# Kernel tuning notes

Hardware: AMD Instinct MI355X
Metric: run time of the kernel (lower is better)

Reference implementation:

```python
import jax, jax.numpy as jnp
import numpy as np

DIM = 1024
D_STATE = 16
D_CONV = 4
EXPAND = 2
D_INNER = EXPAND * DIM          # 2048
DT_RANK = (DIM + 15) // 16      # 64 (math.ceil(d_model/16))
BSZ = 2
SEQ = 2048


def setup_inputs() -> dict:
    key = jax.random.key(0)
    ks = jax.random.split(key, 8)
    g = lambda k, shape, scale: (jax.random.normal(k, shape, jnp.float32) * scale)
    return {
        "x": g(ks[0], (BSZ, SEQ, DIM), 1.0),
        # in_proj: Linear(d_model -> 2*d_inner, bias=False)
        "W_in": g(ks[1], (2 * D_INNER, DIM), DIM ** -0.5),
        # depthwise causal conv1d: groups=d_inner, kernel d_conv, bias=True
        "conv_w": g(ks[2], (D_INNER, 1, D_CONV), D_CONV ** -0.5),
        "conv_b": jnp.zeros((D_INNER,), jnp.float32),
        # x_proj: Linear(d_inner -> dt_rank + 2*d_state, bias=False)
        "W_xproj": g(ks[3], (DT_RANK + 2 * D_STATE, D_INNER), D_INNER ** -0.5),
        # dt_proj: Linear(dt_rank -> d_inner, bias=True)
        "W_dt": g(ks[4], (D_INNER, DT_RANK), DT_RANK ** -0.5),
        "b_dt": g(ks[5], (D_INNER,), 0.1),
        # S4D-real init: A = -exp(A_log), A_log = log(1..d_state)
        "A_log": jnp.log(jnp.broadcast_to(
            jnp.arange(1, D_STATE + 1, dtype=jnp.float32), (D_INNER, D_STATE))),
        "D": jnp.ones((D_INNER,), jnp.float32),
        # out_proj: Linear(d_inner -> d_model, bias=False)
        "W_out": g(ks[6], (DIM, D_INNER), D_INNER ** -0.5),
        # wrapper LayerNorm(dim)
        "gamma": jnp.ones((DIM,), jnp.float32),
        "beta": jnp.zeros((DIM,), jnp.float32),
    }


def reference(x, W_in, conv_w, conv_b, W_xproj, W_dt, b_dt,
              A_log, D, W_out, gamma, beta):
    B, L, _ = x.shape
    # ---- input projection, split into conv path and gate ----
    xz = x @ W_in.T                              # (B, L, 2*d_inner)
    xc, z = jnp.split(xz, 2, axis=-1)
    # ---- depthwise causal conv1d + SiLU ----
    xt = jnp.transpose(xc, (0, 2, 1))            # (B, d_inner, L)
    conv = jax.lax.conv_general_dilated(
        xt, conv_w, window_strides=(1,), padding=[(D_CONV - 1, 0)],
        dimension_numbers=("NCH", "OIH", "NCH"), feature_group_count=D_INNER)
    u = jax.nn.silu(jnp.transpose(conv + conv_b[None, :, None], (0, 2, 1)))  # (B,L,d_inner)
    # ---- input-dependent delta, B, C ----
    xdbc = u @ W_xproj.T                          # (B, L, dt_rank + 2*d_state)
    dt = xdbc[..., :DT_RANK]
    Bm = xdbc[..., DT_RANK:DT_RANK + D_STATE]     # (B, L, d_state)
    Cm = xdbc[..., DT_RANK + D_STATE:]            # (B, L, d_state)
    delta = jax.nn.softplus(dt @ W_dt.T + b_dt)   # (B, L, d_inner)
    A = -jnp.exp(A_log)                           # (d_inner, d_state)
    # ---- selective scan: h_t = exp(dt*A) h_{t-1} + dt*B_t*u_t ; y_t = <h_t, C_t> ----
    def step(h, inputs):
        d_t, u_t, B_t, C_t = inputs               # (B,d_inner),(B,d_inner),(B,S),(B,S)
        dA = jnp.exp(d_t[:, :, None] * A)         # (B, d_inner, S)
        h = h * dA + (d_t * u_t)[:, :, None] * B_t[:, None, :]
        y = jnp.einsum("bds,bs->bd", h, C_t)
        return h, y
    tm = lambda a: jnp.transpose(a, (1, 0, 2))    # time-major for scan
    h0 = jnp.zeros((B, D_INNER, D_STATE), x.dtype)
    _, ys = jax.lax.scan(step, h0, (tm(delta), tm(u), tm(Bm), tm(Cm)))
    y = jnp.transpose(ys, (1, 0, 2)) + u * D      # skip term D*u
    y = y * jax.nn.silu(z)                        # gate
    out = y @ W_out.T                             # (B, L, dim)
    # ---- wrapper LayerNorm(dim), eps=1e-5 ----
    mean = out.mean(-1, keepdims=True)
    var = out.var(-1, keepdims=True)
    return (out - mean) * jax.lax.rsqrt(var + 1e-5) * gamma + beta
```

## Files before the change

### kernel.cpp

```cpp
#include <hip/hip_runtime.h>
#include <stdint.h>

typedef unsigned short u16;
typedef __bf16 bf16x8 __attribute__((ext_vector_type(8)));
typedef unsigned short u16x8 __attribute__((ext_vector_type(8)));
typedef unsigned short u16x4 __attribute__((ext_vector_type(4)));
typedef float f32x4 __attribute__((ext_vector_type(4)));

#define BSZ 2
#define SEQ 2048
#define DIM 1024
#define D_INNER 2048
#define DT_RANK 64
#define D_STATE 16
#define XPROJ_N 96
#define NCHUNK 32
#define CHUNK_T 64
#define LOG2E 1.44269504f

#define N_X   4194304
#define N_W   4194304
#define N_WX  196608
#define N_WDT 131072
#define N_WO  2097152
#define N_XD  393216

__device__ __forceinline__ float bf2f(u16 h) {
    return __uint_as_float(((unsigned)h) << 16);
}
__device__ __forceinline__ u16 f2bf(float f) {
    unsigned u = __float_as_uint(f);
    unsigned r = (u + 0x7FFFu + ((u >> 16) & 1u)) >> 16;
    return (u16)r;
}

__device__ __forceinline__ f32x4 mfma16(bf16x8 a, bf16x8 b, f32x4 c) {
    return __builtin_amdgcn_mfma_f32_16x16x32_bf16(a, b, c, 0, 0, 0);
}

__device__ __forceinline__ void gload_lds16(const void* g, void* l) {
    __builtin_amdgcn_global_load_lds(
        (const __attribute__((address_space(1))) unsigned int*)(uintptr_t)g,
        (__attribute__((address_space(3))) unsigned int*)(uintptr_t)l,
        16, 0, 0);
}

__device__ __forceinline__ void split4(const float* __restrict__ in,
                                       u16* __restrict__ hi, u16* __restrict__ lo,
                                       long i)
{
    f32x4 v = *(const f32x4*)(in + i);
    u16x4 h, l;
    #pragma unroll
    for (int j = 0; j < 4; j++) {
        u16 hh = f2bf(v[j]);
        h[j] = hh;
        l[j] = f2bf(v[j] - bf2f(hh));
    }
    *(u16x4*)(hi + i) = h;
    *(u16x4*)(lo + i) = l;
}

__global__ __launch_bounds__(256)
void megasplit4(const float* __restrict__ x,  u16* __restrict__ xh,  u16* __restrict__ xl,
                const float* __restrict__ w,  u16* __restrict__ wh,  u16* __restrict__ wl,
                const float* __restrict__ wx, u16* __restrict__ wxh, u16* __restrict__ wxl,
                const float* __restrict__ wd, u16* __restrict__ wdh, u16* __restrict__ wdl)
{
    long i = ((long)blockIdx.x * 256 + threadIdx.x) * 4;
    if (i < N_X) { split4(x, xh, xl, i); return; }
    i -= N_X;
    if (i < N_W) { split4(w, wh, wl, i); return; }
    i -= N_W;
    if (i < N_WX) { split4(wx, wxh, wxl, i); return; }
    i -= N_WX;
    if (i < N_WDT) { split4(wd, wdh, wdl, i); }
}

__global__ __launch_bounds__(512, 2)
void gemm256_xz(const u16* __restrict__ xh, const u16* __restrict__ xl,
                const u16* __restrict__ wh, const u16* __restrict__ wl,
                u16* __restrict__ xc, float* __restrict__ z)
{
    __shared__ u16 lds[49152];

    const int tid  = threadIdx.x;
    const int w    = tid >> 6;
    const int lane = tid & 63;
    const int r16  = lane & 15;
    const int quad = lane >> 4;
    const int wr   = w >> 2;
    const int wc   = w & 3;
    const long m0  = (long)blockIdx.y * 256;
    const long n0  = (long)blockIdx.x * 256;

    const int c0 = tid, c1 = tid + 512;
    const int ma0 = c0 >> 2, kc0 = ((c0 & 3) ^ ((ma0 >> 1) & 3)) * 8;
    const int ma1 = c1 >> 2, kc1 = ((c1 & 3) ^ ((ma1 >> 1) & 3)) * 8;
    const int arow0 = ((int)m0 + ma0) * DIM + kc0;
    const int arow1 = ((int)m0 + ma1) * DIM + kc1;
    const int brow0 = ((int)n0 + ma0) * DIM + kc0;
    const int brow1 = ((int)n0 + ma1) * DIM + kc1;

    int caof[8], cbof[4];
    #pragma unroll
    for (int i = 0; i < 8; i++) {
        int m = wr * 128 + i * 16 + r16;
        caof[i] = (m * 4 + (quad ^ ((m >> 1) & 3))) * 8;
    }
    #pragma unroll
    for (int j = 0; j < 4; j++) {
        int n = wc * 64 + j * 16 + r16;
        cbof[j] = (n * 4 + (quad ^ ((n >> 1) & 3))) * 8;
    }

    f32x4 acc[8][4];
    #pragma unroll
    for (int i = 0; i < 8; i++)
        #pragma unroll
        for (int j = 0; j < 4; j++) acc[i][j] = {0.f, 0.f, 0.f, 0.f};

    gload_lds16(xh + arow0,      lds + c0 * 8);
    gload_lds16(xh + arow1,      lds + c1 * 8);
    gload_lds16(wh + brow0,      lds + 24576 + c0 * 8);
    gload_lds16(wh + brow1,      lds + 24576 + c1 * 8);
    gload_lds16(xh + arow0 + 32, lds + 8192 + c0 * 8);
    gload_lds16(xh + arow1 + 32, lds + 8192 + c1 * 8);
    gload_lds16(wh + brow0 + 32, lds + 24576 + 8192 + c0 * 8);
    gload_lds16(wh + brow1 + 32, lds + 24576 + 8192 + c1 * 8);
    asm volatile("s_waitcnt vmcnt(4)" ::: "memory");
    __builtin_amdgcn_s_barrier();

    int kt = 0;
#define XZ_ITER(CUR, SL)                                                      \
  {                                                                           \
    int st = kt + 2; if (st > 95) st = 95;                                    \
    const int ts = st >> 5;                                                   \
    const int kb = (st & 31) * 32;                                            \
    const u16* As = (ts < 2) ? xh : xl;                                       \
    const u16* Bs = (ts == 1) ? wl : wh;                                      \
    const u16* Alds = lds + (CUR) * 8192;                                     \
    const u16* Blds = lds + 24576 + (CUR) * 8192;                             \
      \
    bf16x8 bfr[4], afr[4];                                                    \
    _Pragma("unroll") for (int j = 0; j < 4; j++)                             \
        bfr[j] = *(const bf16x8*)(Blds + cbof[j]);                            \
    _Pragma("unroll") for (int i = 0; i < 4; i++)                             \
        afr[i] = *(const bf16x8*)(Alds + caof[i]);                            \
    gload_lds16(As + arow0 + kb, lds + (SL) * 8192 + c0 * 8);                 \
    gload_lds16(As + arow1 + kb, lds + (SL) * 8192 + c1 * 8);                 \
    __builtin_amdgcn_sched_barrier(0);                                        \
    __builtin_amdgcn_s_barrier();                                             \
    asm volatile("s_waitcnt lgkmcnt(0)" ::: "memory");                        \
    __builtin_amdgcn_sched_barrier(0);                                        \
    __builtin_amdgcn_s_setprio(1);                                            \
    _Pragma("unroll") for (int i = 0; i < 4; i++)                             \
      _Pragma("unroll") for (int j = 0; j < 4; j++)                           \
        acc[i][j] = mfma16(afr[i], bfr[j], acc[i][j]);                        \
    __builtin_amdgcn_s_setprio(0);                                            \
    __builtin_amdgcn_sched_barrier(0);                                        \
    __builtin_amdgcn_s_barrier();                                             \
            \
    bf16x8 af2[4];                                                            \
    _Pragma("unroll") for (int i = 0; i < 4; i++)                             \
        af2[i] = *(const bf16x8*)(Alds + caof[4 + i]);                        \
    gload_lds16(Bs + brow0 + kb, lds + 24576 + (SL) * 8192 + c0 * 8);         \
    gload_lds16(Bs + brow1 + kb, lds + 24576 + (SL) * 8192 + c1 * 8);         \
    __builtin_amdgcn_sched_barrier(0);                                        \
    __builtin_amdgcn_s_barrier();                                             \
    asm volatile("s_waitcnt lgkmcnt(0)" ::: "memory");                        \
    __builtin_amdgcn_sched_barrier(0);                                        \
    __builtin_amdgcn_s_setprio(1);                                            \
    _Pragma("unroll") for (int i = 0; i < 4; i++)                             \
      _Pragma("unroll") for (int j = 0; j < 4; j++)                           \
        acc[4 + i][j] = mfma16(af2[i], bfr[j], acc[4 + i][j]);                \
    __builtin_amdgcn_s_setprio(0);                                            \
    __builtin_amdgcn_sched_barrier(0);                                        \
    asm volatile("s_waitcnt vmcnt(4)" ::: "memory");                          \
    __builtin_amdgcn_s_barrier();                                             \
    kt++;                                                                     \
  }

    #pragma unroll 1
    for (int it = 0; it < 32; it++) {
        XZ_ITER(0, 2)
        XZ_ITER(1, 0)
        XZ_ITER(2, 1)
    }
#undef XZ_ITER

    asm volatile("s_waitcnt vmcnt(0)" ::: "memory");

    const bool isz = (n0 >= 2048);
    #pragma unroll
    for (int i = 0; i < 8; i++) {
        #pragma unroll
        for (int j = 0; j < 4; j++) {
            long col = n0 + wc * 64 + j * 16 + r16;
            #pragma unroll
            for (int r = 0; r < 4; r++) {
                long row = m0 + wr * 128 + i * 16 + quad * 4 + r;
                if (!isz) xc[row * (long)D_INNER + col] = f2bf(acc[i][j][r]);
                else      z[row * (long)D_INNER + (col - D_INNER)] = acc[i][j][r];
            }
        }
    }
}

__global__ __launch_bounds__(256)
void gemm128_sk2(const u16* __restrict__ Ah, int lda,
                 const u16* __restrict__ Bh, const u16* __restrict__ Bl, int ldb,
                 float* __restrict__ OutBase, int ldc, int K0)
{
    __shared__ u16 lds[12288];
    u16* Ah_l = lds;
    u16* Bh_l = lds + 4096;
    u16* Bl_l = lds + 8192;

    const int tid  = threadIdx.x;
    const int w    = tid >> 6;
    const int lane = tid & 63;
    const int r16  = lane & 15;
    const int quad = lane >> 4;
    const int wr   = w >> 1;
    const int wc   = w & 1;
    const long m0  = (long)blockIdx.y * 128;
    const long n0  = (long)blockIdx.x * 128;
    const int kbase = blockIdx.z * K0;
    float* Out = OutBase + (long)blockIdx.z * 4194304;

    const int c0 = w * 64 + lane;
    const int c1 = 256 + c0;
    const int ma0 = c0 >> 2, kca0 = ((c0 & 3) ^ ((ma0 >> 1) & 3)) * 8;
    const int ma1 = c1 >> 2, kca1 = ((c1 & 3) ^ ((ma1 >> 1) & 3)) * 8;

    const u16* Arow0 = Ah + (m0 + ma0) * (long)lda + kbase + kca0;
    const u16* Arow1 = Ah + (m0 + ma1) * (long)lda + kbase + kca1;
    const u16* Brow0 = Bh + (n0 + ma0) * (long)ldb + kbase + kca0;
    const u16* Brow1 = Bh + (n0 + ma1) * (long)ldb + kbase + kca1;
    const u16* Blrow0 = Bl + (n0 + ma0) * (long)ldb + kbase + kca0;
    const u16* Blrow1 = Bl + (n0 + ma1) * (long)ldb + kbase + kca1;

    f32x4 acc[4][4];
    #pragma unroll
    for (int i = 0; i < 4; i++)
        #pragma unroll
        for (int j = 0; j < 4; j++) acc[i][j] = {0.f, 0.f, 0.f, 0.f};

    int caof[4], cbof[4];
    #pragma unroll
    for (int i = 0; i < 4; i++) {
        int m = wr * 64 + i * 16 + r16;
        caof[i] = (m * 4 + (quad ^ ((m >> 1) & 3))) * 8;
        int n = wc * 64 + i * 16 + r16;
        cbof[i] = (n * 4 + (quad ^ ((n >> 1) & 3))) * 8;
    }

    for (int k0 = 0; k0 < K0; k0 += 32) {
        __syncthreads();
        gload_lds16(Arow0 + k0, Ah_l + c0 * 8);
        gload_lds16(Arow1 + k0, Ah_l + c1 * 8);
        gload_lds16(Brow0 + k0, Bh_l + c0 * 8);
        gload_lds16(Brow1 + k0, Bh_l + c1 * 8);
        gload_lds16(Blrow0 + k0, Bl_l + c0 * 8);
        gload_lds16(Blrow1 + k0, Bl_l + c1 * 8);
        __syncthreads();

        bf16x8 fah[4], fbh[4], fbl[4];
        #pragma unroll
        for (int i = 0; i < 4; i++) {
            fah[i] = *(const bf16x8*)(Ah_l + caof[i]);
            fbh[i] = *(const bf16x8*)(Bh_l + cbof[i]);
            fbl[i] = *(const bf16x8*)(Bl_l + cbof[i]);
        }
        #pragma unroll
        for (int i = 0; i < 4; i++) {
            #pragma unroll
            for (int j = 0; j < 4; j++) {
                acc[i][j] = mfma16(fah[i], fbh[j], acc[i][j]);
                acc[i][j] = mfma16(fah[i], fbl[j], acc[i][j]);
            }
        }
    }

    #pragma unroll
    for (int i = 0; i < 4; i++) {
        #pragma unroll
        for (int j = 0; j < 4; j++) {
            long col = n0 + wc * 64 + j * 16 + r16;
            #pragma unroll
            for (int r = 0; r < 4; r++) {
                long row = m0 + wr * 64 + i * 16 + quad * 4 + r;
                Out[row * (long)ldc + col] = acc[i][j][r];
            }
        }
    }
}

__global__ __launch_bounds__(64)
void gemm_dt32(const u16* __restrict__ Ah, const u16* __restrict__ Al, int lda,
               const u16* __restrict__ Bh, const u16* __restrict__ Bl, int ldb,
               float* __restrict__ C, int ldc, const float* __restrict__ bias)
{
    const int lane = threadIdx.x;
    const int r16  = lane & 15;
    const int quad = lane >> 4;
    const long m0 = (long)blockIdx.y * 32;
    const long n0 = (long)blockIdx.x * 32;

    const u16* Ah0 = Ah + (m0 + r16) * (long)lda + quad * 8;
    const u16* Ah1 = Ah0 + 16L * lda;
    const u16* Al0 = Al + (m0 + r16) * (long)lda + quad * 8;
    const u16* Al1 = Al0 + 16L * lda;
    const u16* Bh0 = Bh + (n0 + r16) * (long)ldb + quad * 8;
    const u16* Bh1 = Bh0 + 16L * ldb;
    const u16* Bl0 = Bl + (n0 + r16) * (long)ldb + quad * 8;
    const u16* Bl1 = Bl0 + 16L * ldb;

    f32x4 acc00 = {0,0,0,0}, acc01 = {0,0,0,0}, acc10 = {0,0,0,0}, acc11 = {0,0,0,0};

    #pragma unroll
    for (int k = 0; k < DT_RANK; k += 32) {
        bf16x8 a0h = *(const bf16x8*)(Ah0 + k);
        bf16x8 a1h = *(const bf16x8*)(Ah1 + k);
        bf16x8 a0l = *(const bf16x8*)(Al0 + k);
        bf16x8 a1l = *(const bf16x8*)(Al1 + k);
        bf16x8 b0h = *(const bf16x8*)(Bh0 + k);
        bf16x8 b1h = *(const bf16x8*)(Bh1 + k);
        bf16x8 b0l = *(const bf16x8*)(Bl0 + k);
        bf16x8 b1l = *(const bf16x8*)(Bl1 + k);
        acc00 = mfma16(a0h, b0h, acc00); acc00 = mfma16(a0h, b0l, acc00); acc00 = mfma16(a0l, b0h, acc00);
        acc01 = mfma16(a0h, b1h, acc01); acc01 = mfma16(a0h, b1l, acc01); acc01 = mfma16(a0l, b1h, acc01);
        acc10 = mfma16(a1h, b0h, acc10); acc10 = mfma16(a1h, b0l, acc10); acc10 = mfma16(a1l, b0h, acc10);
        acc11 = mfma16(a1h, b1h, acc11); acc11 = mfma16(a1h, b1l, acc11); acc11 = mfma16(a1l, b1h, acc11);
    }

    #pragma unroll
    for (int i = 0; i < 2; i++) {
        #pragma unroll
        for (int j = 0; j < 2; j++) {
            f32x4 v = (i == 0) ? (j == 0 ? acc00 : acc01) : (j == 0 ? acc10 : acc11);
            long col = n0 + j * 16 + r16;
            #pragma unroll
            for (int r = 0; r < 4; r++) {
                long row = m0 + i * 16 + quad * 4 + r;
                float x = v[r] + bias[col];
                x = (x > 15.f) ? x : log1pf(__expf(x));
                C[row * (long)ldc + col] = x;
            }
        }
    }
}

__global__ __launch_bounds__(64)
void gemm3_skp(const u16* __restrict__ A, int lda,
               const u16* __restrict__ Bh, const u16* __restrict__ Bl, int ldb,
               float* __restrict__ Cpart, int ldc, int K0)
{
    const int lane = threadIdx.x;
    const int r16  = lane & 15;
    const int quad = lane >> 4;
    const long m0 = (long)blockIdx.y * 32;
    const long n0 = (long)blockIdx.x * 32;
    const int kbase = blockIdx.z * K0;
    float* C = Cpart + (long)blockIdx.z * N_XD;

    const u16* Ap0 = A  + (m0 + r16) * (long)lda + quad * 8 + kbase;
    const u16* Ap1 = Ap0 + 16L * lda;
    const u16* Bh0 = Bh + (n0 + r16) * (long)ldb + quad * 8 + kbase;
    const u16* Bh1 = Bh0 + 16L * ldb;
    const u16* Bl0 = Bl + (n0 + r16) * (long)ldb + quad * 8 + kbase;
    const u16* Bl1 = Bl0 + 16L * ldb;

    f32x4 acc00 = {0,0,0,0}, acc01 = {0,0,0,0}, acc10 = {0,0,0,0}, acc11 = {0,0,0,0};

    for (int k = 0; k < K0; k += 32) {
        bf16x8 a0 = *(const bf16x8*)(Ap0 + k);
        bf16x8 a1 = *(const bf16x8*)(Ap1 + k);
        bf16x8 b0h = *(const bf16x8*)(Bh0 + k);
        bf16x8 b1h = *(const bf16x8*)(Bh1 + k);
        bf16x8 b0l = *(const bf16x8*)(Bl0 + k);
        bf16x8 b1l = *(const bf16x8*)(Bl1 + k);
        acc00 = mfma16(a0, b0h, acc00); acc00 = mfma16(a0, b0l, acc00);
        acc01 = mfma16(a0, b1h, acc01); acc01 = mfma16(a0, b1l, acc01);
        acc10 = mfma16(a1, b0h, acc10); acc10 = mfma16(a1, b0l, acc10);
        acc11 = mfma16(a1, b1h, acc11); acc11 = mfma16(a1, b1l, acc11);
    }

    #pragma unroll
    for (int i = 0; i < 2; i++) {
        #pragma unroll
        for (int j = 0; j < 2; j++) {
            f32x4 v = (i == 0) ? (j == 0 ? acc00 : acc01) : (j == 0 ? acc10 : acc11);
            long col = n0 + j * 16 + r16;
            #pragma unroll
            for (int r = 0; r < 4; r++) {
                long row = m0 + i * 16 + quad * 4 + r;
                C[row * (long)ldc + col] = v[r];
            }
        }
    }
}

__global__ __launch_bounds__(256)
void combine3(const float* __restrict__ part, float* __restrict__ xdbc,
              u16* __restrict__ hi, u16* __restrict__ lo)
{
    long i = ((long)blockIdx.x * 256 + threadIdx.x) * 4;
    if (i >= N_XD) return;
    f32x4 s = *(const f32x4*)(part + i);
    #pragma unroll
    for (int j = 1; j < 8; j++) {
        f32x4 p = *(const f32x4*)(part + (long)j * N_XD + i);
        s[0] += p[0]; s[1] += p[1]; s[2] += p[2]; s[3] += p[3];
    }
    *(f32x4*)(xdbc + i) = s;
    u16x4 h, l;
    #pragma unroll
    for (int j = 0; j < 4; j++) {
        u16 hh = f2bf(s[j]);
        h[j] = hh;
        l[j] = f2bf(s[j] - bf2f(hh));
    }
    *(u16x4*)(hi + i) = h;
    *(u16x4*)(lo + i) = l;
}

__global__ __launch_bounds__(256)
void conv_silu(const u16* __restrict__ xc, const float* __restrict__ cw,
               const float* __restrict__ cb, u16* __restrict__ u)
{
    long idx = ((long)blockIdx.x * 256 + threadIdx.x) * 8;
    int t  = (int)((idx >> 11) & 2047);
    int d0 = (int)(idx & 2047);

    bf16x8 xrow[4];
    #pragma unroll
    for (int j = 0; j < 4; j++) {
        int tt = t - 3 + j;
        if (tt >= 0) xrow[j] = *(const bf16x8*)(xc + idx + (long)(j - 3) * D_INNER);
        else         xrow[j] = bf16x8{0,0,0,0,0,0,0,0};
    }
    u16x8 out;
    #pragma unroll
    for (int e = 0; e < 8; e++) {
        int d = d0 + e;
        float acc = cb[d];
        #pragma unroll
        for (int j = 0; j < 4; j++)
            acc += cw[d * 4 + j] * (float)xrow[j][e];
        out[e] = f2bf(acc / (1.f + __expf(-acc)));
    }
    *(u16x8*)(u + idx) = out;
}

__global__ __launch_bounds__(256)
void scan_partA(const float* __restrict__ delta, const u16* __restrict__ u,
                const float* __restrict__ xdbc, const float* __restrict__ A_log,
                float* __restrict__ hbuf, float* __restrict__ sdelta,
                const float* __restrict__ wout, u16* __restrict__ wouth,
                u16* __restrict__ woutl)
{
    const int d = blockIdx.x * 256 + threadIdx.x;
    const int c = blockIdx.y;
    const int b = blockIdx.z;
    const int t0 = c * CHUNK_T;

    float Af[16];
    #pragma unroll
    for (int s = 0; s < 16; s++) Af[s] = -__expf(A_log[d * 16 + s]) * LOG2E;

    float h[16];
    #pragma unroll
    for (int s = 0; s < 16; s++) h[s] = 0.f;
    float sd = 0.f;

    const float* dptr = delta + ((long)b * SEQ + t0) * D_INNER + d;
    const u16*   uptr = u     + ((long)b * SEQ + t0) * D_INNER + d;
    const float* xp   = xdbc  + ((long)b * SEQ + t0) * XPROJ_N;

    for (int t = 0; t < CHUNK_T; t++) {
        float dl = dptr[(long)t * D_INNER];
        float uu = bf2f(uptr[(long)t * D_INNER]);
        f32x4 B0 = *(const f32x4*)(xp + t * XPROJ_N + DT_RANK);
        f32x4 B1 = *(const f32x4*)(xp + t * XPROJ_N + DT_RANK + 4);
        f32x4 B2 = *(const f32x4*)(xp + t * XPROJ_N + DT_RANK + 8);
        f32x4 B3 = *(const f32x4*)(xp + t * XPROJ_N + DT_RANK + 12);
        float Bv[16] = {B0[0],B0[1],B0[2],B0[3], B1[0],B1[1],B1[2],B1[3],
                        B2[0],B2[1],B2[2],B2[3], B3[0],B3[1],B3[2],B3[3]};
        sd += dl;
        float dlu = dl * uu;
        #pragma unroll
        for (int s = 0; s < 16; s++)
            h[s] = h[s] * exp2f(dl * Af[s]) + dlu * Bv[s];
    }

    float* hout = hbuf + ((long)(b * NCHUNK + c) * D_INNER + d) * 16;
    #pragma unroll
    for (int s = 0; s < 16; s++) hout[s] = h[s];
    sdelta[(long)(b * NCHUNK + c) * D_INNER + d] = sd;

    long tidg = (((long)b * NCHUNK + c) * 8 + blockIdx.x) * 256 + threadIdx.x;
    long base = tidg * 16;
    #pragma unroll
    for (int k = 0; k < 4; k++) split4(wout, wouth, woutl, base + 4 * k);
}

__global__ __launch_bounds__(256)
void scan_fixup(float* __restrict__ hbuf, const float* __restrict__ sdelta,
                const float* __restrict__ A_log)
{
    const int idx = blockIdx.x * 256 + threadIdx.x;
    const int ds = idx & (D_INNER * 16 - 1);
    const int b  = idx >> 15;
    const float Af = -__expf(A_log[ds]) * LOG2E;
    float hin = 0.f;
    #pragma unroll 4
    for (int c = 0; c < NCHUNK; c++) {
        long gi = (long)(b * NCHUNK + c) * (D_INNER * 16) + ds;
        float e = hbuf[gi];
        hbuf[gi] = hin;
        float sd = sdelta[(long)(b * NCHUNK + c) * D_INNER + (ds >> 4)];
        hin = e + exp2f(Af * sd) * hin;
    }
}

__global__ __launch_bounds__(256)
void scan_partC(const float* __restrict__ delta, const u16* __restrict__ u,
                const float* __restrict__ xdbc, const float* __restrict__ z,
                const float* __restrict__ A_log, const float* __restrict__ Dp,
                const float* __restrict__ hbuf, u16* __restrict__ y)
{
    const int d = blockIdx.x * 256 + threadIdx.x;
    const int c = blockIdx.y;
    const int b = blockIdx.z;
    const int t0 = c * CHUNK_T;

    float Af[16];
    #pragma unroll
    for (int s = 0; s < 16; s++) Af[s] = -__expf(A_log[d * 16 + s]) * LOG2E;
    const float Dd = Dp[d];

    float h[16];
    const float* hin = hbuf + ((long)(b * NCHUNK + c) * D_INNER + d) * 16;
    #pragma unroll
    for (int s = 0; s < 16; s++) h[s] = hin[s];

    const float* dptr = delta + ((long)b * SEQ + t0) * D_INNER + d;
    const u16*   uptr = u     + ((long)b * SEQ + t0) * D_INNER + d;
    const float* zptr = z     + ((long)b * SEQ + t0) * D_INNER + d;
    const float* xp   = xdbc  + ((long)b * SEQ + t0) * XPROJ_N;
    u16* yptr = y + ((long)b * SEQ + t0) * D_INNER + d;

    for (int t = 0; t < CHUNK_T; t++) {
        float dl = dptr[(long)t * D_INNER];
        float uu = bf2f(uptr[(long)t * D_INNER]);
        float zl = zptr[(long)t * D_INNER];
        f32x4 B0 = *(const f32x4*)(xp + t * XPROJ_N + DT_RANK);
        f32x4 B1 = *(const f32x4*)(xp + t * XPROJ_N + DT_RANK + 4);
        f32x4 B2 = *(const f32x4*)(xp + t * XPROJ_N + DT_RANK + 8);
        f32x4 B3 = *(const f32x4*)(xp + t * XPROJ_N + DT_RANK + 12);
        f32x4 C0 = *(const f32x4*)(xp + t * XPROJ_N + DT_RANK + 16);
        f32x4 C1 = *(const f32x4*)(xp + t * XPROJ_N + DT_RANK + 20);
        f32x4 C2 = *(const f32x4*)(xp + t * XPROJ_N + DT_RANK + 24);
        f32x4 C3 = *(const f32x4*)(xp + t * XPROJ_N + DT_RANK + 28);
        float Bv[16] = {B0[0],B0[1],B0[2],B0[3], B1[0],B1[1],B1[2],B1[3],
                        B2[0],B2[1],B2[2],B2[3], B3[0],B3[1],B3[2],B3[3]};
        float Cv[16] = {C0[0],C0[1],C0[2],C0[3], C1[0],C1[1],C1[2],C1[3],
                        C2[0],C2[1],C2[2],C2[3], C3[0],C3[1],C3[2],C3[3]};
        float dlu = dl * uu;
        float p0 = 0.f, p1 = 0.f, p2 = 0.f, p3 = 0.f;
        #pragma unroll
        for (int s = 0; s < 16; s += 4) {
            h[s]   = h[s]   * exp2f(dl * Af[s])   + dlu * Bv[s];
            h[s+1] = h[s+1] * exp2f(dl * Af[s+1]) + dlu * Bv[s+1];
            h[s+2] = h[s+2] * exp2f(dl * Af[s+2]) + dlu * Bv[s+2];
            h[s+3] = h[s+3] * exp2f(dl * Af[s+3]) + dlu * Bv[s+3];
            p0 += h[s]   * Cv[s];
            p1 += h[s+1] * Cv[s+1];
            p2 += h[s+2] * Cv[s+2];
            p3 += h[s+3] * Cv[s+3];
        }
        float acc = (p0 + p1) + (p2 + p3);
        float sz = zl / (1.f + __expf(-zl));
        float yy = (acc + uu * Dd) * sz;
        yptr[(long)t * D_INNER] = f2bf(yy);
    }
}

__global__ __launch_bounds__(256)
void layernorm_kernel(const float* __restrict__ pa, const float* __restrict__ pb,
                      const float* __restrict__ gamma, const float* __restrict__ beta,
                      float* __restrict__ out)
{
    const long row = blockIdx.x;
    const long base = row * DIM;
    int tid = threadIdx.x;
    float v[4];
    float sum = 0.f, sq = 0.f;
    #pragma unroll
    for (int i = 0; i < 4; i++) {
        long c = base + tid + i * 256;
        v[i] = pa[c] + pb[c];
        sum += v[i];
        sq  += v[i] * v[i];
    }
    #pragma unroll
    for (int off = 1; off < 64; off <<= 1) {
        sum += __shfl_xor(sum, off);
        sq  += __shfl_xor(sq, off);
    }
    __shared__ float ssum[4], ssq[4];
    int w = tid >> 6;
    if ((tid & 63) == 0) { ssum[w] = sum; ssq[w] = sq; }
    __syncthreads();
    float ts = ssum[0] + ssum[1] + ssum[2] + ssum[3];
    float tq = ssq[0] + ssq[1] + ssq[2] + ssq[3];
    float mean = ts * (1.f / DIM);
    float var  = tq * (1.f / DIM) - mean * mean;
    float rstd = rsqrtf(var + 1e-5f);
    float* o = out + base;
    #pragma unroll
    for (int i = 0; i < 4; i++) {
        int c = tid + i * 256;
        o[c] = (v[i] - mean) * rstd * gamma[c] + beta[c];
    }
}

extern "C" void kernel_launch(void* const* d_in, const int* in_sizes, int n_in,
                              void* d_out, int out_size, void* d_ws, size_t ws_size,
                              hipStream_t stream)
{
    const float* x      = (const float*)d_in[0];
    const float* W_in   = (const float*)d_in[1];
    const float* conv_w = (const float*)d_in[2];
    const float* conv_b = (const float*)d_in[3];
    const float* W_xproj= (const float*)d_in[4];
    const float* W_dt   = (const float*)d_in[5];
    const float* b_dt   = (const float*)d_in[6];
    const float* A_log  = (const float*)d_in[7];
    const float* Dv     = (const float*)d_in[8];
    const float* W_out  = (const float*)d_in[9];
    const float* gamma  = (const float*)d_in[10];
    const float* beta   = (const float*)d_in[11];

    char* ws = (char*)d_ws;
    u16*   xc    = (u16*)(ws);
    float* g3p   = (float*)(ws);
    u16*   xdh   = (u16*)(ws + 12582912);
    u16*   xdl   = (u16*)(ws + 14155776);
    float* hbuf  = (float*)(ws);
    u16*   wouth = (u16*)(ws + 8388608);
    u16*   woutl = (u16*)(ws + 12582912);
    float* z     = (float*)(ws + 16777216);
    float* opre  = (float*)(ws + 16777216);
    u16*   u     = (u16*)(ws + 50331648);
    u16*   xh    = (u16*)(ws + 67108864);
    u16*   xl    = (u16*)(ws + 75497472);
    u16*   wh    = (u16*)(ws + 83886080);
    u16*   wl    = (u16*)(ws + 92274688);
    float* delta = (float*)(ws + 67108864);
    float* xdbc  = (float*)(ws + 100663296);
    u16*   wxh   = (u16*)(ws + 102236160);
    u16*   wxl   = (u16*)(ws + 102629376);
    u16*   wdth  = (u16*)(ws + 103022592);
    u16*   wdtl  = (u16*)(ws + 103284736);
    float* sdel  = (float*)(ws + 103546880);
    u16*   yb    = (u16*)d_out;

    megasplit4<<<8512, 256, 0, stream>>>(x, xh, xl, W_in, wh, wl,
                                         W_xproj, wxh, wxl, W_dt, wdth, wdtl);
    gemm256_xz<<<dim3(16, 16), 512, 0, stream>>>(xh, xl, wh, wl, xc, z);
    conv_silu<<<4096, 256, 0, stream>>>(xc, conv_w, conv_b, u);
    gemm3_skp<<<dim3(3, 128, 8), 64, 0, stream>>>(
        u, D_INNER, wxh, wxl, D_INNER, g3p, XPROJ_N, 256);
    combine3<<<384, 256, 0, stream>>>(g3p, xdbc, xdh, xdl);
    gemm_dt32<<<dim3(64, 128), 64, 0, stream>>>(
        xdh, xdl, XPROJ_N, wdth, wdtl, DT_RANK, delta, D_INNER, b_dt);
    scan_partA<<<dim3(8, NCHUNK, BSZ), 256, 0, stream>>>(
        delta, u, xdbc, A_log, hbuf, sdel, W_out, wouth, woutl);
    scan_fixup<<<256, 256, 0, stream>>>(hbuf, sdel, A_log);
    scan_partC<<<dim3(8, NCHUNK, BSZ), 256, 0, stream>>>(delta, u, xdbc, z, A_log, Dv, hbuf, yb);
    gemm128_sk2<<<dim3(8, 32, 2), 256, 0, stream>>>(
        yb, D_INNER, wouth, woutl, D_INNER, opre, DIM, 1024);
    layernorm_kernel<<<4096, 256, 0, stream>>>(
        opre, opre + 4194304, gamma, beta, (float*)d_out);
}
```

Measured before the change: 442.3 us.

## Deepen xz GEMM LDS pipeline to four stages with register-prefetched fragments

The in_proj GEMM moves from a 3-stage to a 4-stage LDS ring buffer, prefetching three K-tiles ahead. It also double-buffers the B fragments and preloads the next tile's A fragments into registers during the current MFMA block, so LDS reads overlap compute. This is meant to hide global-load and LDS latency behind the MFMAs. The cost is 128KB of LDS and more registers, which may drop occupancy from 2 blocks per CU to 1.

```diff
diff --git a/kernel.cpp b/kernel.cpp
--- a/kernel.cpp
+++ b/kernel.cpp
@@ -82,7 +82,7 @@
                 const u16* __restrict__ wh, const u16* __restrict__ wl,
                 u16* __restrict__ xc, float* __restrict__ z)
 {
-    __shared__ u16 lds[49152];
+    __shared__ u16 lds[65536];
 
     const int tid  = threadIdx.x;
     const int w    = tid >> 6;
@@ -122,74 +122,82 @@
 
     gload_lds16(xh + arow0,      lds + c0 * 8);
     gload_lds16(xh + arow1,      lds + c1 * 8);
-    gload_lds16(wh + brow0,      lds + 24576 + c0 * 8);
-    gload_lds16(wh + brow1,      lds + 24576 + c1 * 8);
+    gload_lds16(wh + brow0,      lds + 32768 + c0 * 8);
+    gload_lds16(wh + brow1,      lds + 32768 + c1 * 8);
     gload_lds16(xh + arow0 + 32, lds + 8192 + c0 * 8);
     gload_lds16(xh + arow1 + 32, lds + 8192 + c1 * 8);
-    gload_lds16(wh + brow0 + 32, lds + 24576 + 8192 + c0 * 8);
-    gload_lds16(wh + brow1 + 32, lds + 24576 + 8192 + c1 * 8);
-    asm volatile("s_waitcnt vmcnt(4)" ::: "memory");
+    gload_lds16(wh + brow0 + 32, lds + 32768 + 8192 + c0 * 8);
+    gload_lds16(wh + brow1 + 32, lds + 32768 + 8192 + c1 * 8);
+    gload_lds16(xh + arow0 + 64, lds + 16384 + c0 * 8);
+    gload_lds16(xh + arow1 + 64, lds + 16384 + c1 * 8);
+    gload_lds16(wh + brow0 + 64, lds + 32768 + 16384 + c0 * 8);
+    gload_lds16(wh + brow1 + 64, lds + 32768 + 16384 + c1 * 8);
+    asm volatile("s_waitcnt vmcnt(8)" ::: "memory");
     __builtin_amdgcn_s_barrier();
 
+    bf16x8 aA[4], aB[4], bE[4], bO[4];
+    #pragma unroll
+    for (int j = 0; j < 4; j++) bE[j] = *(const bf16x8*)(lds + 32768 + cbof[j]);
+    #pragma unroll
+    for (int i = 0; i < 4; i++) aA[i] = *(const bf16x8*)(lds + caof[i]);
+
     int kt = 0;
-#define XZ_ITER(CUR, SL)                                                      \
+#define TILE_STEP(SC, SN, SS, BC, BN)                                         \
   {                                                                           \
-    int st = kt + 2; if (st > 95) st = 95;                                    \
+    int st = kt + 3; if (st > 95) st = 95;                                    \
     const int ts = st >> 5;                                                   \
     const int kb = (st & 31) * 32;                                            \
     const u16* As = (ts < 2) ? xh : xl;                                       \
     const u16* Bs = (ts == 1) ? wl : wh;                                      \
-    const u16* Alds = lds + (CUR) * 8192;                                     \
-    const u16* Blds = lds + 24576 + (CUR) * 8192;                             \
-      \
-    bf16x8 bfr[4], afr[4];                                                    \
-    _Pragma("unroll") for (int j = 0; j < 4; j++)                             \
-        bfr[j] = *(const bf16x8*)(Blds + cbof[j]);                            \
+    const u16* Ac = lds + (SC) * 8192;                                        \
+    const u16* An = lds + (SN) * 8192;                                        \
+    const u16* Bn = lds + 32768 + (SN) * 8192;                                \
+        \
+    asm volatile("s_waitcnt lgkmcnt(0)" ::: "memory");                        \
+    __builtin_amdgcn_sched_barrier(0);                                        \
     _Pragma("unroll") for (int i = 0; i < 4; i++)                             \
-        afr[i] = *(const bf16x8*)(Alds + caof[i]);                            \
-    gload_lds16(As + arow0 + kb, lds + (SL) * 8192 + c0 * 8);                 \
-    gload_lds16(As + arow1 + kb, lds + (SL) * 8192 + c1 * 8);                 \
-    __builtin_amdgcn_sched_barrier(0);                                        \
-    __builtin_amdgcn_s_barrier();                                             \
-    asm volatile("s_waitcnt lgkmcnt(0)" ::: "memory");                        \
+        aB[i] = *(const bf16x8*)(Ac + caof[4 + i]);                           \
+    gload_lds16(As + arow0 + kb, lds + (SS) * 8192 + c0 * 8);                 \
+    gload_lds16(As + arow1 + kb, lds + (SS) * 8192 + c1 * 8);                 \
     __builtin_amdgcn_sched_barrier(0);                                        \
     __builtin_amdgcn_s_setprio(1);                                            \
     _Pragma("unroll") for (int i = 0; i < 4; i++)                             \
       _Pragma("unroll") for (int j = 0; j < 4; j++)                           \
-        acc[i][j] = mfma16(afr[i], bfr[j], acc[i][j]);                        \
+        acc[i][j] = mfma16(aA[i], BC[j], acc[i][j]);                          \
     __builtin_amdgcn_s_setprio(0);                                            \
     __builtin_amdgcn_sched_barrier(0);                                        \
+    asm volatile("s_waitcnt vmcnt(6)" ::: "memory");                          \
     __builtin_amdgcn_s_barrier();                                             \
-            \
-    bf16x8 af2[4];                                                            \
+     \
+    asm volatile("s_waitcnt lgkmcnt(0)" ::: "memory");                        \
+    __builtin_amdgcn_sched_barrier(0);                                        \
+    _Pragma("unroll") for (int j = 0; j < 4; j++)                             \
+        BN[j] = *(const bf16x8*)(Bn + cbof[j]);                               \
     _Pragma("unroll") for (int i = 0; i < 4; i++)                             \
-        af2[i] = *(const bf16x8*)(Alds + caof[4 + i]);                        \
-    gload_lds16(Bs + brow0 + kb, lds + 24576 + (SL) * 8192 + c0 * 8);         \
-    gload_lds16(Bs + brow1 + kb, lds + 24576 + (SL) * 8192 + c1 * 8);         \
-    __builtin_amdgcn_sched_barrier(0);                                        \
-    __builtin_amdgcn_s_barrier();                                             \
-    asm volatile("s_waitcnt lgkmcnt(0)" ::: "memory");                        \
+        aA[i] = *(const bf16x8*)(An + caof[i]);                               \
+    gload_lds16(Bs + brow0 + kb, lds + 32768 + (SS) * 8192 + c0 * 8);         \
+    gload_lds16(Bs + brow1 + kb, lds + 32768 + (SS) * 8192 + c1 * 8);         \
     __builtin_amdgcn_sched_barrier(0);                                        \
     __builtin_amdgcn_s_setprio(1);                                            \
     _Pragma("unroll") for (int i = 0; i < 4; i++)                             \
       _Pragma("unroll") for (int j = 0; j < 4; j++)                           \
-        acc[4 + i][j] = mfma16(af2[i], bfr[j], acc[4 + i][j]);                \
+        acc[4 + i][j] = mfma16(aB[i], BC[j], acc[4 + i][j]);                  \
     __builtin_amdgcn_s_setprio(0);                                            \
     __builtin_amdgcn_sched_barrier(0);                                        \
-    asm volatile("s_waitcnt vmcnt(4)" ::: "memory");                          \
     __builtin_amdgcn_s_barrier();                                             \
     kt++;                                                                     \
   }
 
     #pragma unroll 1
-    for (int it = 0; it < 32; it++) {
-        XZ_ITER(0, 2)
-        XZ_ITER(1, 0)
-        XZ_ITER(2, 1)
-    }
-#undef XZ_ITER
-
-    asm volatile("s_waitcnt vmcnt(0)" ::: "memory");
+    for (int it = 0; it < 24; it++) {
+        TILE_STEP(0, 1, 3, bE, bO)
+        TILE_STEP(1, 2, 0, bO, bE)
+        TILE_STEP(2, 3, 1, bE, bO)
+        TILE_STEP(3, 0, 2, bO, bE)
+    }
+#undef TILE_STEP
+
+    asm volatile("s_waitcnt vmcnt(0) lgkmcnt(0)" ::: "memory");
 
     const bool isz = (n0 >= 2048);
     #pragma unroll
```

Measured after the change: 443.6 us. Within noise of the previous version (+0.3%).

## Replace out-projection GEMM with pipelined 256x256 tile kernel, four-way split

Applied to the files above, without the earlier changes.

Replaces the 128x128 two-way split-K out-projection GEMM with a 256x256 tile kernel of 512 threads using a triple-buffered LDS pipeline. It has interleaved barriers and raised MFMA priority, modeled on the in-projection kernel. The hi and lo weight halves are now separate grid slices rather than two MFMAs per step, giving four partial outputs. LayerNorm sums all four partials. This aims to improve operand reuse and overlap loads with MFMA, at the cost of extra partial-buffer traffic and workspace size.

```diff
diff --git a/kernel.cpp b/kernel.cpp
--- a/kernel.cpp
+++ b/kernel.cpp
@@ -207,91 +207,129 @@
     }
 }
 
-__global__ __launch_bounds__(256)
-void gemm128_sk2(const u16* __restrict__ Ah, int lda,
-                 const u16* __restrict__ Bh, const u16* __restrict__ Bl, int ldb,
-                 float* __restrict__ OutBase, int ldc, int K0)
-{
-    __shared__ u16 lds[12288];
-    u16* Ah_l = lds;
-    u16* Bh_l = lds + 4096;
-    u16* Bl_l = lds + 8192;
+__global__ __launch_bounds__(512, 2)
+void gemm256_out(const u16* __restrict__ A, const u16* __restrict__ Bh,
+                 const u16* __restrict__ Bl, float* __restrict__ OutBase)
+{
+    __shared__ u16 lds[49152];
 
     const int tid  = threadIdx.x;
     const int w    = tid >> 6;
     const int lane = tid & 63;
     const int r16  = lane & 15;
     const int quad = lane >> 4;
-    const int wr   = w >> 1;
-    const int wc   = w & 1;
-    const long m0  = (long)blockIdx.y * 128;
-    const long n0  = (long)blockIdx.x * 128;
-    const int kbase = blockIdx.z * K0;
-    float* Out = OutBase + (long)blockIdx.z * 4194304;
-
-    const int c0 = w * 64 + lane;
-    const int c1 = 256 + c0;
-    const int ma0 = c0 >> 2, kca0 = ((c0 & 3) ^ ((ma0 >> 1) & 3)) * 8;
-    const int ma1 = c1 >> 2, kca1 = ((c1 & 3) ^ ((ma1 >> 1) & 3)) * 8;
-
-    const u16* Arow0 = Ah + (m0 + ma0) * (long)lda + kbase + kca0;
-    const u16* Arow1 = Ah + (m0 + ma1) * (long)lda + kbase + kca1;
-    const u16* Brow0 = Bh + (n0 + ma0) * (long)ldb + kbase + kca0;
-    const u16* Brow1 = Bh + (n0 + ma1) * (long)ldb + kbase + kca1;
-    const u16* Blrow0 = Bl + (n0 + ma0) * (long)ldb + kbase + kca0;
-    const u16* Blrow1 = Bl + (n0 + ma1) * (long)ldb + kbase + kca1;
-
-    f32x4 acc[4][4];
-    #pragma unroll
-    for (int i = 0; i < 4; i++)
+    const int wr   = w >> 2;
+    const int wc   = w & 3;
+    const long m0  = (long)blockIdx.y * 256;
+    const long n0  = (long)blockIdx.x * 256;
+    const int  kz  = blockIdx.z;
+    const u16* Bs  = (kz >= 2) ? Bl : Bh;
+    const int  kbase = (kz & 1) * 1024;
+    float* Out = OutBase + (long)kz * 4194304;
+
+    const int c0 = tid, c1 = tid + 512;
+    const int ma0 = c0 >> 2, kc0 = ((c0 & 3) ^ ((ma0 >> 1) & 3)) * 8;
+    const int ma1 = c1 >> 2, kc1 = ((c1 & 3) ^ ((ma1 >> 1) & 3)) * 8;
+    const int arow0 = ((int)m0 + ma0) * D_INNER + kbase + kc0;
+    const int arow1 = ((int)m0 + ma1) * D_INNER + kbase + kc1;
+    const int brow0 = ((int)n0 + ma0) * D_INNER + kbase + kc0;
+    const int brow1 = ((int)n0 + ma1) * D_INNER + kbase + kc1;
+
+    int caof[8], cbof[4];
+    #pragma unroll
+    for (int i = 0; i < 8; i++) {
+        int m = wr * 128 + i * 16 + r16;
+        caof[i] = (m * 4 + (quad ^ ((m >> 1) & 3))) * 8;
+    }
+    #pragma unroll
+    for (int j = 0; j < 4; j++) {
+        int n = wc * 64 + j * 16 + r16;
+        cbof[j] = (n * 4 + (quad ^ ((n >> 1) & 3))) * 8;
+    }
+
+    f32x4 acc[8][4];
+    #pragma unroll
+    for (int i = 0; i < 8; i++)
         #pragma unroll
         for (int j = 0; j < 4; j++) acc[i][j] = {0.f, 0.f, 0.f, 0.f};
 
-    int caof[4], cbof[4];
-    #pragma unroll
-    for (int i = 0; i < 4; i++) {
-        int m = wr * 64 + i * 16 + r16;
-        caof[i] = (m * 4 + (quad ^ ((m >> 1) & 3))) * 8;
-        int n = wc * 64 + i * 16 + r16;
-        cbof[i] = (n * 4 + (quad ^ ((n >> 1) & 3))) * 8;
-    }
-
-    for (int k0 = 0; k0 < K0; k0 += 32) {
-        __syncthreads();
-        gload_lds16(Arow0 + k0, Ah_l + c0 * 8);
-        gload_lds16(Arow1 + k0, Ah_l + c1 * 8);
-        gload_lds16(Brow0 + k0, Bh_l + c0 * 8);
-        gload_lds16(Brow1 + k0, Bh_l + c1 * 8);
-        gload_lds16(Blrow0 + k0, Bl_l + c0 * 8);
-        gload_lds16(Blrow1 + k0, Bl_l + c1 * 8);
-        __syncthreads();
-
-        bf16x8 fah[4], fbh[4], fbl[4];
-        #pragma unroll
-        for (int i = 0; i < 4; i++) {
-            fah[i] = *(const bf16x8*)(Ah_l + caof[i]);
-            fbh[i] = *(const bf16x8*)(Bh_l + cbof[i]);
-            fbl[i] = *(const bf16x8*)(Bl_l + cbof[i]);
-        }
-        #pragma unroll
-        for (int i = 0; i < 4; i++) {
-            #pragma unroll
-            for (int j = 0; j < 4; j++) {
-                acc[i][j] = mfma16(fah[i], fbh[j], acc[i][j]);
-                acc[i][j] = mfma16(fah[i], fbl[j], acc[i][j]);
-            }
-        }
-    }
-
-    #pragma unroll
-    for (int i = 0; i < 4; i++) {
+    gload_lds16(A  + arow0,      lds + c0 * 8);
+    gload_lds16(A  + arow1,      lds + c1 * 8);
+    gload_lds16(Bs + brow0,      lds + 24576 + c0 * 8);
+    gload_lds16(Bs + brow1,      lds + 24576 + c1 * 8);
+    gload_lds16(A  + arow0 + 32, lds + 8192 + c0 * 8);
+    gload_lds16(A  + arow1 + 32, lds + 8192 + c1 * 8);
+    gload_lds16(Bs + brow0 + 32, lds + 24576 + 8192 + c0 * 8);
+    gload_lds16(Bs + brow1 + 32, lds + 24576 + 8192 + c1 * 8);
+    asm volatile("s_waitcnt vmcnt(4)" ::: "memory");
+    __builtin_amdgcn_s_barrier();
+
+    int kt = 0;
+#define OUT_ITER(CUR, SL)                                                     \
+  {                                                                           \
+    int st = kt + 2; if (st > 31) st = 31;                                    \
+    const int kb = st * 32;                                                   \
+    const u16* Alds = lds + (CUR) * 8192;                                     \
+    const u16* Blds = lds + 24576 + (CUR) * 8192;                             \
+    bf16x8 bfr[4], afr[4];                                                    \
+    _Pragma("unroll") for (int j = 0; j < 4; j++)                             \
+        bfr[j] = *(const bf16x8*)(Blds + cbof[j]);                            \
+    _Pragma("unroll") for (int i = 0; i < 4; i++)                             \
+        afr[i] = *(const bf16x8*)(Alds + caof[i]);                            \
+    gload_lds16(A + arow0 + kb, lds + (SL) * 8192 + c0 * 8);                  \
+    gload_lds16(A + arow1 + kb, lds + (SL) * 8192 + c1 * 8);                  \
+    __builtin_amdgcn_sched_barrier(0);                                        \
+    __builtin_amdgcn_s_barrier();                                             \
+    asm volatile("s_waitcnt lgkmcnt(0)" ::: "memory");                        \
+    __builtin_amdgcn_sched_barrier(0);                                        \
+    __builtin_amdgcn_s_setprio(1);                                            \
+    _Pragma("unroll") for (int i = 0; i < 4; i++)                             \
+      _Pragma("unroll") for (int j = 0; j < 4; j++)                           \
+        acc[i][j] = mfma16(afr[i], bfr[j], acc[i][j]);                        \
+    __builtin_amdgcn_s_setprio(0);                                            \
+    __builtin_amdgcn_sched_barrier(0);                                        \
+    __builtin_amdgcn_s_barrier();                                             \
+    bf16x8 af2[4];                                                            \
+    _Pragma("unroll") for (int i = 0; i < 4; i++)                             \
+        af2[i] = *(const bf16x8*)(Alds + caof[4 + i]);                        \
+    gload_lds16(Bs + brow0 + kb, lds + 24576 + (SL) * 8192 + c0 * 8);         \
+    gload_lds16(Bs + brow1 + kb, lds + 24576 + (SL) * 8192 + c1 * 8);         \
+    __builtin_amdgcn_sched_barrier(0);                                        \
+    __builtin_amdgcn_s_barrier();                                             \
+    asm volatile("s_waitcnt lgkmcnt(0)" ::: "memory");                        \
+    __builtin_amdgcn_sched_barrier(0);                                        \
+    __builtin_amdgcn_s_setprio(1);                                            \
+    _Pragma("unroll") for (int i = 0; i < 4; i++)                             \
+      _Pragma("unroll") for (int j = 0; j < 4; j++)                           \
+        acc[4 + i][j] = mfma16(af2[i], bfr[j], acc[4 + i][j]);                \
+    __builtin_amdgcn_s_setprio(0);                                            \
+    __builtin_amdgcn_sched_barrier(0);                                        \
+    asm volatile("s_waitcnt vmcnt(4)" ::: "memory");                          \
+    __builtin_amdgcn_s_barrier();                                             \
+    kt++;                                                                     \
+  }
+
+    #pragma unroll 1
+    for (int it = 0; it < 10; it++) {
+        OUT_ITER(0, 2)
+        OUT_ITER(1, 0)
+        OUT_ITER(2, 1)
+    }
+    OUT_ITER(0, 2)
+    OUT_ITER(1, 0)
+#undef OUT_ITER
+
+    asm volatile("s_waitcnt vmcnt(0)" ::: "memory");
+
+    #pragma unroll
+    for (int i = 0; i < 8; i++) {
         #pragma unroll
         for (int j = 0; j < 4; j++) {
             long col = n0 + wc * 64 + j * 16 + r16;
             #pragma unroll
             for (int r = 0; r < 4; r++) {
-                long row = m0 + wr * 64 + i * 16 + quad * 4 + r;
-                Out[row * (long)ldc + col] = acc[i][j][r];
+                long row = m0 + wr * 128 + i * 16 + quad * 4 + r;
+                Out[row * (long)DIM + col] = acc[i][j][r];
             }
         }
     }
@@ -589,7 +627,7 @@
 }
 
 __global__ __launch_bounds__(256)
-void layernorm_kernel(const float* __restrict__ pa, const float* __restrict__ pb,
+void layernorm_kernel(const float* __restrict__ p0,
                       const float* __restrict__ gamma, const float* __restrict__ beta,
                       float* __restrict__ out)
 {
@@ -601,7 +639,7 @@
     #pragma unroll
     for (int i = 0; i < 4; i++) {
         long c = base + tid + i * 256;
-        v[i] = pa[c] + pb[c];
+        v[i] = (p0[c] + p0[c + 4194304]) + (p0[c + 8388608] + p0[c + 12582912]);
         sum += v[i];
         sq  += v[i] * v[i];
     }
@@ -681,8 +719,6 @@
         delta, u, xdbc, A_log, hbuf, sdel, W_out, wouth, woutl);
     scan_fixup<<<256, 256, 0, stream>>>(hbuf, sdel, A_log);
     scan_partC<<<dim3(8, NCHUNK, BSZ), 256, 0, stream>>>(delta, u, xdbc, z, A_log, Dv, hbuf, yb);
-    gemm128_sk2<<<dim3(8, 32, 2), 256, 0, stream>>>(
-        yb, D_INNER, wouth, woutl, D_INNER, opre, DIM, 1024);
-    layernorm_kernel<<<4096, 256, 0, stream>>>(
-        opre, opre + 4194304, gamma, beta, (float*)d_out);
-}
+    gemm256_out<<<dim3(4, 16, 4), 512, 0, stream>>>(yb, wouth, woutl, opre);
+    layernorm_kernel<<<4096, 256, 0, stream>>>(opre, gamma, beta, (float*)d_out);
+}
```

New measurement: 440.2 us. Within noise of the previous version (-0.5%).
